# Kernel optimization log

Hardware: AMD Instinct MI355X
Metric: run time of the kernel (lower is better)

Reference implementation:

```python
import jax, jax.numpy as jnp
import numpy as np

NUM_HEADS = 16
HEAD_DIM = 64
ROPE_BASE = 160000.0


def _rope_tables(seq_len, head_dim):
    inv_freq = 1.0 / (ROPE_BASE ** (jnp.arange(0, head_dim, 2, dtype=jnp.float32) / head_dim))
    freqs = jnp.arange(seq_len, dtype=jnp.float32)[:, None] * inv_freq[None, :]  # [S, hd/2]
    return jnp.cos(freqs)[None, None], jnp.sin(freqs)[None, None]  # [1,1,S,hd/2]


def _apply_rope(x, cos, sin):
    # x: [B, nh, S, hd]; split-half rotation as in the torch module
    x1, x2 = jnp.split(x, 2, axis=-1)
    return jnp.concatenate([x1 * cos - x2 * sin, x2 * cos + x1 * sin], axis=-1)


def setup_inputs() -> dict:
    key = jax.random.key(0)
    k1, k2, k3 = jax.random.split(key, 3)
    B, S, H = 2, 2048, 1024
    hidden_states = jax.random.normal(k1, (B, S, H), dtype=jnp.float32)
    # additive causal mask: 0 for allowed, -1e9 for future positions
    causal = jnp.tril(jnp.ones((S, S), dtype=bool))
    attention_mask = jnp.where(causal, 0.0, -1e9).astype(jnp.float32)[None, None]
    Wqkv = jax.random.normal(k2, (H, 3 * H), dtype=jnp.float32) * (H ** -0.5)
    Wo = jax.random.normal(k3, (H, H), dtype=jnp.float32) * (H ** -0.5)
    return {"hidden_states": hidden_states, "attention_mask": attention_mask, "Wqkv": Wqkv, "Wo": Wo}


def reference(hidden_states, attention_mask, Wqkv, Wo):
    B, S, H = hidden_states.shape
    nh, hd = NUM_HEADS, HEAD_DIM
    scale = hd ** -0.5

    qkv = hidden_states @ Wqkv                                   # [B,S,3H]
    qkv = qkv.reshape(B, S, 3, nh, hd).transpose(2, 0, 3, 1, 4)  # [3,B,nh,S,hd]
    q, k, v = qkv[0], qkv[1], qkv[2]

    cos, sin = _rope_tables(S, hd)
    q = _apply_rope(q, cos, sin)
    k = _apply_rope(k, cos, sin)

    scores = jnp.einsum('bhqd,bhkd->bhqk', q, k) * scale + attention_mask
    attn = jax.nn.softmax(scores, axis=-1)
    out = jnp.einsum('bhqk,bhkd->bhqd', attn, v)                 # [B,nh,S,hd]
    out = out.transpose(0, 2, 1, 3).reshape(B, S, H)
    return out @ Wo
```

## Files before the change

kernel.cpp:

```cpp
#include <hip/hip_runtime.h>
#include <hip/hip_bf16.h>

typedef __bf16 bf16x8 __attribute__((ext_vector_type(8)));
typedef float f32x4 __attribute__((ext_vector_type(4)));
typedef unsigned short u16;

__device__ __forceinline__ u16 f2bf(float f) {
    union { float f; unsigned u; } x{f};
    unsigned r = x.u + 0x7fffu + ((x.u >> 16) & 1u);
    return (u16)(r >> 16);
}
__device__ __forceinline__ unsigned pk2(float a, float b) {
    union { float f; unsigned u; } x{a}, y{b};
    return ((x.u + 0x8000u) >> 16) | ((y.u + 0x8000u) & 0xffff0000u);
}
__device__ __forceinline__ float ex2(float x) { return __builtin_amdgcn_exp2f(x); }
__device__ __forceinline__ f32x4 zero4() { f32x4 z = {0.f, 0.f, 0.f, 0.f}; return z; }

typedef const __attribute__((address_space(1))) unsigned int* gp1_t;
typedef __attribute__((address_space(3))) unsigned int* lp3_t;
__device__ __forceinline__ void async16(const u16* g, u16* l) {
    __builtin_amdgcn_global_load_lds((gp1_t)g, (lp3_t)l, 16, 0, 0);
}

__global__ void __launch_bounds__(256) prep(const float* __restrict__ hs,
                                            u16* __restrict__ Xb,
                                            const float* __restrict__ Wqkv,
                                            u16* __restrict__ Wqkvt,
                                            const float* __restrict__ Wo,
                                            u16* __restrict__ Wot,
                                            float* __restrict__ cosT,
                                            float* __restrict__ sinT) {
    __shared__ float tile[32][33];
    const int blk = blockIdx.x, t = threadIdx.x;
    if (blk < 4096) {
        int i = (blk * 256 + t) * 4;
        float4 v = *(const float4*)(hs + i);
        ushort4 o;
        o.x = f2bf(v.x); o.y = f2bf(v.y); o.z = f2bf(v.z); o.w = f2bf(v.w);
        *(ushort4*)(Xb + i) = o;
    } else if (blk < 8192) {
        const float* W; u16* Wt; int N, bx, by;
        bool qkv = (blk < 7168);
        if (qkv) { int bid = blk - 4096; W = Wqkv; Wt = Wqkvt; N = 3072; bx = bid % 96; by = bid / 96; }
        else     { int bid = blk - 7168; W = Wo;   Wt = Wot;   N = 1024; bx = bid % 32; by = bid / 32; }
        const int K = 1024;
        int tx = t & 31, ty = t >> 5;
        int n0 = bx * 32, k0 = by * 32;
#pragma unroll
        for (int i = 0; i < 32; i += 8)
            tile[ty + i][tx] = W[(size_t)(k0 + ty + i) * N + n0 + tx];
        __syncthreads();
#pragma unroll
        for (int i = 0; i < 32; i += 8) {
            int n = n0 + ty + i;
            int np = n;
            if (qkv) {
                int hh = (n >> 6) & 3, f = (n >> 4) & 3;
                np = (n & ~255) | (((f >> 1) * 8 + hh * 2 + (f & 1)) << 4) | (n & 15);
            }
            Wt[(size_t)np * K + k0 + tx] = f2bf(tile[tx][ty + i]);
        }
    } else {
        int idx = (blk - 8192) * 256 + t;
        int d = idx & 31, s = idx >> 5;
        float inv = expf(-(float)d * 0.374466538f);
        float th = (float)s * inv;
        cosT[idx] = cosf(th);
        sinT[idx] = sinf(th);
    }
}

struct GemmCtx {
    f32x4 acc[4][4];
    int m16, q4, wm, wn;
};
template <int KDIM>
__device__ __forceinline__ void gemm_loop(const u16* __restrict__ A,
                                          const u16* __restrict__ Bt,
                                          int bm, int bn, GemmCtx& cx,
                                          u16* As, u16* Bs) {
    const int t = threadIdx.x;
    const int lane = t & 63, w = t >> 6;
    cx.wm = w >> 1; cx.wn = w & 1;
    cx.m16 = lane & 15; cx.q4 = lane >> 4;

    const int lrow = lane >> 2;
    const int kchunk = (lane & 3) ^ ((lane >> 3) & 3);
    const u16* Ag = A + (size_t)(bm * 128 + w * 32 + lrow) * KDIM + kchunk * 8;
    const u16* Bg = Bt + (size_t)(bn * 128 + w * 32 + lrow) * KDIM + kchunk * 8;
    const int l0 = (w * 32) * 32;
    const int l1 = (w * 32 + 16) * 32;
    const int kswz = (cx.q4 ^ ((cx.m16 >> 1) & 3)) * 8;

#pragma unroll
    for (int i = 0; i < 4; i++)
#pragma unroll
        for (int j = 0; j < 4; j++) cx.acc[i][j] = zero4();

    constexpr int NT = KDIM / 32;
    async16(Ag, As + l0);
    async16(Ag + 16 * KDIM, As + l1);
    async16(Bg, Bs + l0);
    async16(Bg + 16 * KDIM, Bs + l1);
    async16(Ag + 32, As + 4096 + l0);
    async16(Ag + 16 * KDIM + 32, As + 4096 + l1);
    async16(Bg + 32, Bs + 4096 + l0);
    async16(Bg + 16 * KDIM + 32, Bs + 4096 + l1);

    int co = 0, po = 2 * 4096;
#pragma unroll 1
    for (int tt = 0; tt < NT; ++tt) {
        if (tt + 1 < NT) {
            asm volatile("s_waitcnt vmcnt(4)" ::: "memory");
        } else {
            asm volatile("s_waitcnt vmcnt(0)" ::: "memory");
        }
        __builtin_amdgcn_s_barrier();
        __builtin_amdgcn_sched_barrier(0);
        if (tt + 2 < NT) {
            const int k0 = (tt + 2) * 32;
            async16(Ag + k0, As + po + l0);
            async16(Ag + 16 * KDIM + k0, As + po + l1);
            async16(Bg + k0, Bs + po + l0);
            async16(Bg + 16 * KDIM + k0, Bs + po + l1);
        }
        __builtin_amdgcn_sched_barrier(0);

        bf16x8 af[4], bf[4];
#pragma unroll
        for (int i = 0; i < 4; i++)
            af[i] = *(const bf16x8*)&As[co + (cx.wm * 64 + i * 16 + cx.m16) * 32 + kswz];
#pragma unroll
        for (int j = 0; j < 4; j++)
            bf[j] = *(const bf16x8*)&Bs[co + (cx.wn * 64 + j * 16 + cx.m16) * 32 + kswz];
#pragma unroll
        for (int i = 0; i < 4; i++)
#pragma unroll
            for (int j = 0; j < 4; j++)
                cx.acc[i][j] = __builtin_amdgcn_mfma_f32_16x16x32_bf16(af[i], bf[j], cx.acc[i][j], 0, 0, 0);

        asm volatile("" ::: "memory");
        __builtin_amdgcn_sched_barrier(0);
        co += 4096; if (co == 12288) co = 0;
        po += 4096; if (po == 12288) po = 0;
    }
}

__global__ void __launch_bounds__(512, 2) gemm_qkv(const u16* __restrict__ A,
                                                   const u16* __restrict__ Bt,
                                                   const float* __restrict__ cosT,
                                                   const float* __restrict__ sinT,
                                                   u16* __restrict__ Q,
                                                   u16* __restrict__ Kd,
                                                   u16* __restrict__ Vt) {
    __shared__ __align__(16) u16 As[2 * 256 * 64];
    __shared__ __align__(16) u16 Bs[2 * 256 * 64];
    constexpr int HB = 256 * 64;
    const int t = threadIdx.x, lane = t & 63, w = t >> 6;
    const int wm = w >> 2, wn = w & 3;
    const int m16 = lane & 15, q4 = lane >> 4, m7 = m16 & 7;
    const int hw = blockIdx.x;
    const int orig = (hw & 7) * 24 + (hw >> 3);
    const int bm = orig / 12, bn = orig % 12;

    const int srow = lane >> 3;
    const int schunk = (lane & 7) ^ srow;
    const u16* Ag = A + (size_t)(bm * 256 + w * 8 + srow) * 1024 + schunk * 8;
    const u16* Bg = Bt + (size_t)(bn * 256 + w * 8 + srow) * 1024 + schunk * 8;
    u16* AsW = As + w * 512;
    u16* BsW = Bs + w * 512;

    f32x4 acc[8][4];
#pragma unroll
    for (int i = 0; i < 8; i++)
#pragma unroll
        for (int j = 0; j < 4; j++) acc[i][j] = zero4();

    const int slt0 = (q4 ^ m7) * 8;
    const int slt1 = ((4 + q4) ^ m7) * 8;

#define STGA(S, H) do { const u16* g_ = Ag + (size_t)(H) * 131072 + (S) * 64; \
    u16* l_ = AsW + ((S) & 1) * HB + (H) * 8192; \
    async16(g_, l_); async16(g_ + 65536, l_ + 4096); } while (0)
#define STGB(S, H) do { const u16* g_ = Bg + (size_t)(H) * 131072 + (S) * 64; \
    u16* l_ = BsW + ((S) & 1) * HB + (H) * 8192; \
    async16(g_, l_); async16(g_ + 65536, l_ + 4096); } while (0)

    STGA(0, 0); STGB(0, 0); STGA(0, 1); STGB(0, 1); STGA(1, 0); STGB(1, 0);
    asm volatile("s_waitcnt vmcnt(4)" ::: "memory");
    __builtin_amdgcn_sched_barrier(0);
    __builtin_amdgcn_s_barrier();

#define MFMA8(IB, B0, B1) do { \
    _Pragma("unroll") for (int i4 = 0; i4 < 4; i4++) \
    _Pragma("unroll") for (int j2 = 0; j2 < 2; j2++) \
        acc[(IB) + i4][(JB) + j2] = __builtin_amdgcn_mfma_f32_16x16x32_bf16(a0[i4], B0[j2], acc[(IB) + i4][(JB) + j2], 0, 0, 0); \
    _Pragma("unroll") for (int i4 = 0; i4 < 4; i4++) \
    _Pragma("unroll") for (int j2 = 0; j2 < 2; j2++) \
        acc[(IB) + i4][(JB) + j2] = __builtin_amdgcn_mfma_f32_16x16x32_bf16(a1[i4], B1[j2], acc[(IB) + i4][(JB) + j2], 0, 0, 0); \
} while (0)

#define BAR1() do { __builtin_amdgcn_sched_barrier(0); __builtin_amdgcn_s_barrier(); \
                    __builtin_amdgcn_s_setprio(1); } while (0)
#define BAR2() do { __builtin_amdgcn_s_setprio(0); asm volatile("" ::: "memory"); \
                    __builtin_amdgcn_sched_barrier(0); __builtin_amdgcn_s_barrier(); } while (0)

#pragma unroll 1
    for (int T = 0; T < 16; ++T) {
        const int co = (T & 1) * HB;
        const int aL = co + (wm * 64 + m16) * 64;
        const int aH = aL + 128 * 64;
        const int bL = co + (wn * 32 + m16) * 64;
        const int bH = bL + 128 * 64;
        bf16x8 a0[4], a1[4], pl0[2], pl1[2], ph0[2], ph1[2];

#pragma unroll
        for (int i4 = 0; i4 < 4; i4++) {
            a0[i4] = *(const bf16x8*)&As[aL + i4 * 1024 + slt0];
            a1[i4] = *(const bf16x8*)&As[aL + i4 * 1024 + slt1];
        }
#pragma unroll
        for (int j2 = 0; j2 < 2; j2++) {
            pl0[j2] = *(const bf16x8*)&Bs[bL + j2 * 1024 + slt0];
            pl1[j2] = *(const bf16x8*)&Bs[bL + j2 * 1024 + slt1];
        }
        if (T < 15) STGA(T + 1, 1);
        BAR1();
        { constexpr int JB = 0; MFMA8(0, pl0, pl1); }
        BAR2();

#pragma unroll
        for (int j2 = 0; j2 < 2; j2++) {
            ph0[j2] = *(const bf16x8*)&Bs[bH + j2 * 1024 + slt0];
            ph1[j2] = *(const bf16x8*)&Bs[bH + j2 * 1024 + slt1];
        }
        if (T < 15) STGB(T + 1, 1);
        BAR1();
        { constexpr int JB = 2; MFMA8(0, ph0, ph1); }
        BAR2();

#pragma unroll
        for (int i4 = 0; i4 < 4; i4++) {
            a0[i4] = *(const bf16x8*)&As[aH + i4 * 1024 + slt0];
            a1[i4] = *(const bf16x8*)&As[aH + i4 * 1024 + slt1];
        }
        if (T < 14) STGA(T + 2, 0);
        BAR1();
        { constexpr int JB = 0; MFMA8(4, pl0, pl1); }
        BAR2();

        if (T < 14) {
            STGB(T + 2, 0);
            asm volatile("s_waitcnt vmcnt(4)" ::: "memory");
        } else {
            asm volatile("s_waitcnt vmcnt(0)" ::: "memory");
        }
        BAR1();
        { constexpr int JB = 2; MFMA8(4, ph0, ph1); }
        BAR2();
    }
#undef STGA
#undef STGB
#undef MFMA8
#undef BAR1
#undef BAR2

    const int colbase = bn * 256 + wn * 64;
    const int type = colbase >> 10;
    const int h = (colbase & 1023) >> 6;

    if (type == 2) {
#pragma unroll
        for (int i = 0; i < 8; i++) {
            int sr = bm * 256 + (i >> 2) * 128 + wm * 64 + (i & 3) * 16 + q4 * 4;
            int b = sr >> 11, sl = sr & 2047;
            size_t ob = (size_t)(b * 16 + h) * 64 * 2048;
#pragma unroll
            for (int j = 0; j < 4; j++) {
                int d = j * 16 + m16;
                ushort4 o;
                o.x = f2bf(acc[i][j][0]);
                o.y = f2bf(acc[i][j][1]);
                o.z = f2bf(acc[i][j][2]);
                o.w = f2bf(acc[i][j][3]);
                *(ushort4*)&Vt[ob + (size_t)d * 2048 + sl] = o;
            }
        }
    } else {
        u16* dst = (type == 0) ? Q : Kd;
        const float qs = (type == 0) ? 0.1803368801f  : 1.0f;
#pragma unroll
        for (int i = 0; i < 8; i++)
#pragma unroll
            for (int rr = 0; rr < 4; rr++) {
                int r = bm * 256 + (i >> 2) * 128 + wm * 64 + (i & 3) * 16 + q4 * 4 + rr;
                int b = r >> 11, s = r & 2047;
                size_t ob = ((size_t)((b * 16 + h) * 2048 + s)) * 64;
#pragma unroll
                for (int j2 = 0; j2 < 2; j2++) {
                    int d = j2 * 16 + m16;
                    float cs = cosT[s * 32 + d];
                    float sn = sinT[s * 32 + d];
                    float x1 = acc[i][j2][rr];
                    float x2 = acc[i][j2 + 2][rr];
                    dst[ob + d]      = f2bf((x1 * cs - x2 * sn) * qs);
                    dst[ob + d + 32] = f2bf((x2 * cs + x1 * sn) * qs);
                }
            }
    }
}

__global__ void __launch_bounds__(256) gemm_out(const u16* __restrict__ A,
                                                const u16* __restrict__ Bt,
                                                float* __restrict__ C) {
    __shared__ __align__(16) u16 As[3 * 128 * 32];
    __shared__ __align__(16) u16 Bs[3 * 128 * 32];
    GemmCtx cx;
    const int bm = blockIdx.y, bn = blockIdx.x;
    gemm_loop<1024>(A, Bt, bm, bn, cx, As, Bs);
    const int N = 1024;
#pragma unroll
    for (int i = 0; i < 4; i++)
#pragma unroll
        for (int j = 0; j < 4; j++)
#pragma unroll
            for (int rr = 0; rr < 4; rr++) {
                int row = bm * 128 + cx.wm * 64 + i * 16 + cx.q4 * 4 + rr;
                int col = bn * 128 + cx.wn * 64 + j * 16 + cx.m16;
                C[(size_t)row * N + col] = cx.acc[i][j][rr];
            }
}

__global__ void __launch_bounds__(512) attn_kernel(const u16* __restrict__ Q,
                                                   const u16* __restrict__ Kg_,
                                                   const u16* __restrict__ Vtg_,
                                                   u16* __restrict__ O) {
    __shared__ __align__(16) u16 Ks[2][64][72];
    __shared__ __align__(16) u16 Vs[2][64][72];
    __shared__ __align__(16) u16 Pt[8][16][72];
    const int t = threadIdx.x, w = t >> 6;
    const int m16 = t & 15, q4 = (t & 63) >> 4;
    const int bx = blockIdx.x, bh = blockIdx.y;
    const size_t base = (size_t)bh * 2048 * 64;
    const int b = bh >> 4, h = bh & 15;
    const int skey = t >> 3, sc = (t & 7) * 8;

#pragma unroll 1
    for (int ph = 0; ph < 2; ph++) {
        const int st = ph ? (15 - bx) : bx;
        const int qrow = st * 128 + w * 16 + m16;
        const u16* Qg = Q + base + (size_t)qrow * 64;
        bf16x8 qf0 = *(const bf16x8*)(Qg + q4 * 8);
        bf16x8 qf1 = *(const bf16x8*)(Qg + 32 + q4 * 8);

        f32x4 occ[4];
#pragma unroll
        for (int dc = 0; dc < 4; dc++) occ[dc] = zero4();
        float li = 0.f;

        const int jtmax = 2 * st + 1;
        const int jd = 2 * st + (w >> 2);

        const u16* Kb0 = Kg_ + base + skey * 64 + sc;
        const u16* Vt0 = Vtg_ + base + (size_t)skey * 2048 + sc;
        uint4 ka = *(const uint4*)(Kb0);
        uint4 va = *(const uint4*)(Vt0);

#pragma unroll 1
        for (int jt = 0; jt <= jtmax; jt++) {
            const int bi = jt & 1;
            *(uint4*)&Ks[bi][skey][sc] = ka;
            *(uint4*)&Vs[bi][skey][sc] = va;
            if (jt < jtmax) {
                ka = *(const uint4*)(Kb0 + (size_t)(jt + 1) * 4096);
                va = *(const uint4*)(Vt0 + (size_t)(jt + 1) * 64);
            }
            __syncthreads();

            if (jt <= jd) {
                f32x4 stv[4];
#pragma unroll
                for (int c = 0; c < 4; c++) stv[c] = zero4();
#pragma unroll
                for (int c = 0; c < 4; c++) {
                    bf16x8 kf0 = *(const bf16x8*)&Ks[bi][c * 16 + m16][q4 * 8];
                    bf16x8 kf1 = *(const bf16x8*)&Ks[bi][c * 16 + m16][32 + q4 * 8];
                    stv[c] = __builtin_amdgcn_mfma_f32_16x16x32_bf16(kf0, qf0, stv[c], 0, 0, 0);
                    stv[c] = __builtin_amdgcn_mfma_f32_16x16x32_bf16(kf1, qf1, stv[c], 0, 0, 0);
                }

                float pv[4][4];
#pragma unroll
                for (int c = 0; c < 4; c++)
#pragma unroll
                    for (int rr = 0; rr < 4; rr++) pv[c][rr] = stv[c][rr];
                if (jt == jd) {
                    const int ql = qrow - 64 * jt;
#pragma unroll
                    for (int c = 0; c < 4; c++)
#pragma unroll
                        for (int rr = 0; rr < 4; rr++)
                            if (c * 16 + q4 * 4 + rr > ql) pv[c][rr] = -1e30f;
                }

#pragma unroll
                for (int c = 0; c < 4; c++) {
                    float p0 = ex2(pv[c][0] - 24.f);
                    float p1 = ex2(pv[c][1] - 24.f);
                    float p2 = ex2(pv[c][2] - 24.f);
                    float p3 = ex2(pv[c][3] - 24.f);
                    li += (p0 + p1) + (p2 + p3);
                    *(uint2*)&Pt[w][m16][c * 16 + q4 * 4] = make_uint2(pk2(p0, p1), pk2(p2, p3));
                }

#pragma unroll
                for (int ks = 0; ks < 2; ks++) {
                    bf16x8 pf = *(const bf16x8*)&Pt[w][m16][ks * 32 + q4 * 8];
#pragma unroll
                    for (int dc = 0; dc < 4; dc++) {
                        bf16x8 vf = *(const bf16x8*)&Vs[bi][dc * 16 + m16][ks * 32 + q4 * 8];
                        occ[dc] = __builtin_amdgcn_mfma_f32_16x16x32_bf16(vf, pf, occ[dc], 0, 0, 0);
                    }
                }
            }
        }

        li += __shfl_xor(li, 16);
        li += __shfl_xor(li, 32);
        float rli = 1.0f / li;
        u16* Op = O + ((size_t)(b * 2048 + qrow)) * 1024 + h * 64 + q4 * 4;
#pragma unroll
        for (int dc = 0; dc < 4; dc++) {
            ushort4 o;
            o.x = f2bf(occ[dc][0] * rli);
            o.y = f2bf(occ[dc][1] * rli);
            o.z = f2bf(occ[dc][2] * rli);
            o.w = f2bf(occ[dc][3] * rli);
            *(ushort4*)(Op + dc * 16) = o;
        }
        __syncthreads();
    }
}

extern "C" void kernel_launch(void* const* d_in, const int* in_sizes, int n_in,
                              void* d_out, int out_size, void* d_ws, size_t ws_size,
                              hipStream_t stream) {
    const float* hs   = (const float*)d_in[0];
    const float* Wqkv = (const float*)d_in[2];
    const float* Wo   = (const float*)d_in[3];
    float* out = (float*)d_out;

    const int BS = 4096;
    const int H = 1024, N3 = 3072;
    const int SH = 32 * 2048 * 64;

    u16* Xb    = (u16*)d_ws;
    u16* Wqkvt = Xb + (size_t)BS * H;
    u16* Wot   = Wqkvt + (size_t)N3 * H;
    u16* Qb    = Wot + (size_t)H * H;
    u16* Kb    = Qb + SH;
    u16* Vtb   = Kb + SH;
    u16* AOb   = Vtb + SH;
    float* cosT = (float*)(AOb + (size_t)BS * H);
    float* sinT = cosT + 2048 * 32;

    prep<<<8448, 256, 0, stream>>>(hs, Xb, Wqkv, Wqkvt, Wo, Wot, cosT, sinT);

    gemm_qkv<<<192, 512, 0, stream>>>(Xb, Wqkvt, cosT, sinT, Qb, Kb, Vtb);

    attn_kernel<<<dim3(8, 32), 512, 0, stream>>>(Qb, Kb, Vtb, AOb);

    gemm_out<<<dim3(H / 128, BS / 128), 256, 0, stream>>>(AOb, Wot, out);
}
```

Measured before the change: 189.5 us.

## Restructure attention to split keys across warps with XOR-swizzled LDS tiles

The attention kernel moves from 8 warps that each own 16 query rows to 4 warps (256 threads) that each own 16 keys of the 64-key tile for all 128 queries. P is written into a shared 128-row tile and then re-read so each warp computes PV for its own 32 queries. Row sums are combined across warps through shared memory. K/V/P tiles use XOR swizzling instead of padding to avoid bank conflicts. This adds a second barrier per key tile, applies the mask on both diagonal tiles for all warps, uses more registers for Q fragments, and writes the output with scalar stores.

After: 210.8 us. 11.3% more time.

```diff
diff --git a/kernel.cpp b/kernel.cpp
--- a/kernel.cpp
+++ b/kernel.cpp
@@ -332,113 +332,133 @@
             }
 }
 
-__global__ void __launch_bounds__(512) attn_kernel(const u16* __restrict__ Q,
+__global__ void __launch_bounds__(256) attn_kernel(const u16* __restrict__ Q,
                                                    const u16* __restrict__ Kg_,
                                                    const u16* __restrict__ Vtg_,
                                                    u16* __restrict__ O) {
-    __shared__ __align__(16) u16 Ks[2][64][72];
-    __shared__ __align__(16) u16 Vs[2][64][72];
-    __shared__ __align__(16) u16 Pt[8][16][72];
-    const int t = threadIdx.x, w = t >> 6;
-    const int m16 = t & 15, q4 = (t & 63) >> 4;
+    __shared__ __align__(16) u16 Ks[2][64][64];
+    __shared__ __align__(16) u16 Vs[2][64][64];
+    __shared__ __align__(16) u16 Pt[128][72];
+    __shared__ float Li[4][128];
+    const int t = threadIdx.x, w = t >> 6, lane = t & 63;
+    const int m16 = lane & 15, q4 = lane >> 4, m7 = m16 & 7;
     const int bx = blockIdx.x, bh = blockIdx.y;
     const size_t base = (size_t)bh * 2048 * 64;
     const int b = bh >> 4, h = bh & 15;
-    const int skey = t >> 3, sc = (t & 7) * 8;
+    const int kr = t >> 2, kc = t & 3;
+    const int wg0 = (kc ^ (kr & 7)) * 8;
+    const int wg1 = ((kc + 4) ^ (kr & 7)) * 8;
 
 #pragma unroll 1
     for (int ph = 0; ph < 2; ph++) {
         const int st = ph ? (15 - bx) : bx;
-        const int qrow = st * 128 + w * 16 + m16;
-        const u16* Qg = Q + base + (size_t)qrow * 64;
-        bf16x8 qf0 = *(const bf16x8*)(Qg + q4 * 8);
-        bf16x8 qf1 = *(const bf16x8*)(Qg + 32 + q4 * 8);
-
-        f32x4 occ[4];
-#pragma unroll
-        for (int dc = 0; dc < 4; dc++) occ[dc] = zero4();
-        float li = 0.f;
+        bf16x8 qf[8][2];
+        const u16* Qg = Q + base + (size_t)(st * 128 + m16) * 64 + q4 * 8;
+#pragma unroll
+        for (int qb = 0; qb < 8; qb++) {
+            qf[qb][0] = *(const bf16x8*)(Qg + qb * 16 * 64);
+            qf[qb][1] = *(const bf16x8*)(Qg + qb * 16 * 64 + 32);
+        }
+
+        f32x4 occ[2][4];
+#pragma unroll
+        for (int qb2 = 0; qb2 < 2; qb2++)
+#pragma unroll
+            for (int db = 0; db < 4; db++) occ[qb2][db] = zero4();
+        float li[8];
+#pragma unroll
+        for (int qb = 0; qb < 8; qb++) li[qb] = 0.f;
 
         const int jtmax = 2 * st + 1;
-        const int jd = 2 * st + (w >> 2);
-
-        const u16* Kb0 = Kg_ + base + skey * 64 + sc;
-        const u16* Vt0 = Vtg_ + base + (size_t)skey * 2048 + sc;
-        uint4 ka = *(const uint4*)(Kb0);
-        uint4 va = *(const uint4*)(Vt0);
+        const u16* Kb0 = Kg_ + base + (size_t)kr * 64 + kc * 8;
+        const u16* Vb0 = Vtg_ + base + (size_t)kr * 2048 + kc * 8;
+        uint4 ka0 = *(const uint4*)(Kb0);
+        uint4 ka1 = *(const uint4*)(Kb0 + 32);
+        uint4 va0 = *(const uint4*)(Vb0);
+        uint4 va1 = *(const uint4*)(Vb0 + 32);
 
 #pragma unroll 1
         for (int jt = 0; jt <= jtmax; jt++) {
             const int bi = jt & 1;
-            *(uint4*)&Ks[bi][skey][sc] = ka;
-            *(uint4*)&Vs[bi][skey][sc] = va;
+            *(uint4*)&Ks[bi][kr][wg0] = ka0;
+            *(uint4*)&Ks[bi][kr][wg1] = ka1;
+            *(uint4*)&Vs[bi][kr][wg0] = va0;
+            *(uint4*)&Vs[bi][kr][wg1] = va1;
             if (jt < jtmax) {
-                ka = *(const uint4*)(Kb0 + (size_t)(jt + 1) * 4096);
-                va = *(const uint4*)(Vt0 + (size_t)(jt + 1) * 64);
+                const u16* kn = Kb0 + (size_t)(jt + 1) * 4096;
+                const u16* vn = Vb0 + (jt + 1) * 64;
+                ka0 = *(const uint4*)(kn);
+                ka1 = *(const uint4*)(kn + 32);
+                va0 = *(const uint4*)(vn);
+                va1 = *(const uint4*)(vn + 32);
             }
             __syncthreads();
 
-            if (jt <= jd) {
-                f32x4 stv[4];
-#pragma unroll
-                for (int c = 0; c < 4; c++) stv[c] = zero4();
-#pragma unroll
-                for (int c = 0; c < 4; c++) {
-                    bf16x8 kf0 = *(const bf16x8*)&Ks[bi][c * 16 + m16][q4 * 8];
-                    bf16x8 kf1 = *(const bf16x8*)&Ks[bi][c * 16 + m16][32 + q4 * 8];
-                    stv[c] = __builtin_amdgcn_mfma_f32_16x16x32_bf16(kf0, qf0, stv[c], 0, 0, 0);
-                    stv[c] = __builtin_amdgcn_mfma_f32_16x16x32_bf16(kf1, qf1, stv[c], 0, 0, 0);
+            bf16x8 kf0 = *(const bf16x8*)&Ks[bi][w * 16 + m16][(q4 ^ m7) * 8];
+            bf16x8 kf1 = *(const bf16x8*)&Ks[bi][w * 16 + m16][((4 + q4) ^ m7) * 8];
+            const int keyb = 64 * jt + 16 * w + 4 * q4;
+            const bool dm = (jt >= 2 * st);
+            const int pg = (2 * w + (q4 >> 1)) ^ m7;
+            const int po = pg * 8 + (q4 & 1) * 4;
+#pragma unroll
+            for (int qb = 0; qb < 8; qb++) {
+                f32x4 stv = zero4();
+                stv = __builtin_amdgcn_mfma_f32_16x16x32_bf16(kf0, qf[qb][0], stv, 0, 0, 0);
+                stv = __builtin_amdgcn_mfma_f32_16x16x32_bf16(kf1, qf[qb][1], stv, 0, 0, 0);
+                const int qg = st * 128 + qb * 16 + m16;
+                float p[4];
+#pragma unroll
+                for (int rr = 0; rr < 4; rr++) {
+                    float s = stv[rr];
+                    if (dm && (keyb + rr > qg)) s = -1e30f;
+                    p[rr] = ex2(s - 24.f);
                 }
-
-                float pv[4][4];
-#pragma unroll
-                for (int c = 0; c < 4; c++)
-#pragma unroll
-                    for (int rr = 0; rr < 4; rr++) pv[c][rr] = stv[c][rr];
-                if (jt == jd) {
-                    const int ql = qrow - 64 * jt;
-#pragma unroll
-                    for (int c = 0; c < 4; c++)
-#pragma unroll
-                        for (int rr = 0; rr < 4; rr++)
-                            if (c * 16 + q4 * 4 + rr > ql) pv[c][rr] = -1e30f;
-                }
-
-#pragma unroll
-                for (int c = 0; c < 4; c++) {
-                    float p0 = ex2(pv[c][0] - 24.f);
-                    float p1 = ex2(pv[c][1] - 24.f);
-                    float p2 = ex2(pv[c][2] - 24.f);
-                    float p3 = ex2(pv[c][3] - 24.f);
-                    li += (p0 + p1) + (p2 + p3);
-                    *(uint2*)&Pt[w][m16][c * 16 + q4 * 4] = make_uint2(pk2(p0, p1), pk2(p2, p3));
-                }
-
-#pragma unroll
-                for (int ks = 0; ks < 2; ks++) {
-                    bf16x8 pf = *(const bf16x8*)&Pt[w][m16][ks * 32 + q4 * 8];
-#pragma unroll
-                    for (int dc = 0; dc < 4; dc++) {
-                        bf16x8 vf = *(const bf16x8*)&Vs[bi][dc * 16 + m16][ks * 32 + q4 * 8];
-                        occ[dc] = __builtin_amdgcn_mfma_f32_16x16x32_bf16(vf, pf, occ[dc], 0, 0, 0);
-                    }
-                }
-            }
-        }
-
-        li += __shfl_xor(li, 16);
-        li += __shfl_xor(li, 32);
-        float rli = 1.0f / li;
-        u16* Op = O + ((size_t)(b * 2048 + qrow)) * 1024 + h * 64 + q4 * 4;
-#pragma unroll
-        for (int dc = 0; dc < 4; dc++) {
-            ushort4 o;
-            o.x = f2bf(occ[dc][0] * rli);
-            o.y = f2bf(occ[dc][1] * rli);
-            o.z = f2bf(occ[dc][2] * rli);
-            o.w = f2bf(occ[dc][3] * rli);
-            *(ushort4*)(Op + dc * 16) = o;
-        }
+                li[qb] += (p[0] + p[1]) + (p[2] + p[3]);
+                *(uint2*)&Pt[qb * 16 + m16][po] = make_uint2(pk2(p[0], p[1]), pk2(p[2], p[3]));
+            }
+            __syncthreads();
+
+#pragma unroll
+            for (int kh = 0; kh < 2; kh++) {
+                const int gs = ((kh * 4 + q4) ^ m7) * 8;
+                bf16x8 pf[2], vf[4];
+#pragma unroll
+                for (int qb2 = 0; qb2 < 2; qb2++)
+                    pf[qb2] = *(const bf16x8*)&Pt[w * 32 + qb2 * 16 + m16][gs];
+#pragma unroll
+                for (int db = 0; db < 4; db++)
+                    vf[db] = *(const bf16x8*)&Vs[bi][db * 16 + m16][gs];
+#pragma unroll
+                for (int qb2 = 0; qb2 < 2; qb2++)
+#pragma unroll
+                    for (int db = 0; db < 4; db++)
+                        occ[qb2][db] = __builtin_amdgcn_mfma_f32_16x16x32_bf16(pf[qb2], vf[db], occ[qb2][db], 0, 0, 0);
+            }
+        }
+
+#pragma unroll
+        for (int qb = 0; qb < 8; qb++) {
+            li[qb] += __shfl_xor(li[qb], 16);
+            li[qb] += __shfl_xor(li[qb], 32);
+        }
+        if (lane < 16) {
+#pragma unroll
+            for (int qb = 0; qb < 8; qb++) Li[w][qb * 16 + m16] = li[qb];
+        }
+        __syncthreads();
+
+#pragma unroll
+        for (int qb2 = 0; qb2 < 2; qb2++)
+#pragma unroll
+            for (int rr = 0; rr < 4; rr++) {
+                int ql = w * 32 + qb2 * 16 + q4 * 4 + rr;
+                float rli = 1.0f / (Li[0][ql] + Li[1][ql] + Li[2][ql] + Li[3][ql]);
+                int qgl = st * 128 + ql;
+                u16* Op = O + ((size_t)(b * 2048 + qgl)) * 1024 + h * 64 + m16;
+#pragma unroll
+                for (int db = 0; db < 4; db++)
+                    Op[db * 16] = f2bf(occ[qb2][db][rr] * rli);
+            }
         __syncthreads();
     }
 }
@@ -469,7 +489,7 @@
 
     gemm_qkv<<<192, 512, 0, stream>>>(Xb, Wqkvt, cosT, sinT, Qb, Kb, Vtb);
 
-    attn_kernel<<<dim3(8, 32), 512, 0, stream>>>(Qb, Kb, Vtb, AOb);
+    attn_kernel<<<dim3(8, 32), 256, 0, stream>>>(Qb, Kb, Vtb, AOb);
 
     gemm_out<<<dim3(H / 128, BS / 128), 256, 0, stream>>>(AOb, Wot, out);
 }
```
